# Performance work log

Hardware: AMD Instinct MI355X
Metric: run time of the kernel (lower is better)

Reference implementation:

```python
import jax, jax.numpy as jnp
import numpy as np

N_TOKENS = 100000
UNITS = 150  # CustomizeLSTMCell.TRANSITION_STATE_OUTPUTS_DIM


def setup_inputs() -> dict:
    key = jax.random.key(0)
    ks = jax.random.split(key, 9)
    f = lambda k, shape: jax.random.normal(k, shape, dtype=jnp.float32)
    return {
        "s_in": f(ks[0], (N_TOKENS, UNITS)),
        "s_out": f(ks[1], (N_TOKENS, UNITS)),
        "h_in": f(ks[2], (N_TOKENS, UNITS)),
        "h_out": f(ks[3], (N_TOKENS, UNITS)),
        "last_c": f(ks[4], (N_TOKENS, UNITS)),
        "w_in_input": f(ks[5], (UNITS, UNITS)) * 0.05,
        "w_out_input": f(ks[6], (UNITS, UNITS)) * 0.05,
        "u_in_input": f(ks[7], (UNITS, UNITS)) * 0.05,
        "u_out_input": f(ks[8], (UNITS, UNITS)) * 0.05,
    }


def reference(s_in, s_out, h_in, h_out, last_c,
              w_in_input, w_out_input, u_in_input, u_out_input):
    # Faithful to the source: all four gates use the *_input weights and no bias
    # (the original call() computes identical pre-activations for every gate).
    pre = (s_in @ w_in_input + s_out @ w_out_input
           + h_in @ u_in_input + h_out @ u_out_input)  # [N, H]
    gate = jax.nn.sigmoid(pre)
    # input_gate == output_gate == forget_gate == update_gate == gate
    cell_state = gate * last_c + gate * gate
    hidden_state = gate * jnp.tanh(cell_state)
    return hidden_state, cell_state
```

## Files before the change

### kernel.cpp

```cpp
#include <hip/hip_runtime.h>
#include <hip/hip_bf16.h>

typedef __attribute__((ext_vector_type(8))) short short8;
typedef __attribute__((ext_vector_type(4))) float f32x4;

#define NTOK   100000
#define H      150
#define NKS    20
#define BM     64
#define LBUF   18432
#define OUTOFF (NTOK * H)
#define AS1 __attribute__((address_space(1)))
#define AS3 __attribute__((address_space(3)))

__device__ __forceinline__ unsigned short f2bf(float f) {
    unsigned int u = __builtin_bit_cast(unsigned int, f);
    u = (u + 0x7FFFu + ((u >> 16) & 1u)) >> 16;
    return (unsigned short)u;
}

template<int N> __device__ __forceinline__ void vwait() {
    if constexpr (N == 6)       asm volatile("s_waitcnt vmcnt(6)" ::: "memory");
    else if constexpr (N == 4)  asm volatile("s_waitcnt vmcnt(4)" ::: "memory");
    else if constexpr (N == 23) asm volatile("s_waitcnt vmcnt(23)" ::: "memory");
    else if constexpr (N == 22) asm volatile("s_waitcnt vmcnt(22)" ::: "memory");
    else if constexpr (N == 20) asm volatile("s_waitcnt vmcnt(20)" ::: "memory");
    else                        asm volatile("s_waitcnt vmcnt(0)" ::: "memory");
}

__global__ void prep_w(const float* __restrict__ w_in, const float* __restrict__ w_out,
                       const float* __restrict__ u_in, const float* __restrict__ u_out,
                       unsigned short* __restrict__ wb) {
    int idx = blockIdx.x * 256 + threadIdx.x;
    if (idx >= NKS * 10 * 512) return;
    int j    = idx & 7;
    int lane = (idx >> 3) & 63;
    int n    = (idx >> 9) % 10;
    int ks   = idx / 5120;
    int seg  = ks / 5, s5 = ks % 5;
    int col  = n * 16 + (lane & 15);
    int p    = (lane >> 4) * 8 + j;
    int k2   = (s5 < 4) ? (s5 * 32 + p) : (118 + p);
    float v = 0.0f;
    if (col < H && !(s5 == 4 && p < 10)) {
        const float* W = (seg == 0) ? w_in : (seg == 1) ? w_out : (seg == 2) ? u_in : u_out;
        v = W[k2 * H + col];
    }
    wb[idx] = f2bf(v);
}

__global__ __launch_bounds__(512, 4) void lstm_fused(
        const float* __restrict__ s_in, const float* __restrict__ s_out,
        const float* __restrict__ h_in, const float* __restrict__ h_out,
        const float* __restrict__ last_c, const unsigned short* __restrict__ wb,
        float* __restrict__ out) {
    __shared__ __align__(16) char lds[4 * LBUF];

    const int t     = threadIdx.x;
    const int lane  = t & 63;
    const int wid   = t >> 6;
    const int waveM = wid >> 1;
    const int waveN = wid & 1;
    const int lrow  = lane & 15;
    const int lko   = lane >> 4;
    const int r0blk = blockIdx.x * BM;
    const bool cw3  = (wid < 2);

    const float* Xseg[4] = {s_in, s_out, h_in, h_out};

    f32x4 acc[5];
#pragma unroll
    for (int n = 0; n < 5; n++) acc[n] = (f32x4){0.f, 0.f, 0.f, 0.f};

    float lcv[4][5];

    auto stage = [&](int ks2) {
        char* lb = &lds[(ks2 & 3) * LBUF];
        const int s5 = ks2 % 5;
        const int sofs = (s5 < 4) ? s5 * 128 : 472;
        {
            const char* xb = (const char*)Xseg[ks2 / 5];
            int rowg = r0blk + wid * 8 + (lane >> 3);
            if (rowg > NTOK - 1) rowg = NTOK - 1;
            const int q = (lane & 7) ^ ((lane >> 3) & 7);
            const long go = (long)rowg * 600 + sofs + q * 16;
            __builtin_amdgcn_global_load_lds(
                (const AS1 void*)(xb + go),
                (AS3 void*)(lb + wid * 1024 + lane * 16), 16, 0, 0);
        }
        {
            const char* bsrc = (const char*)wb + (long)ks2 * 10240;
            __builtin_amdgcn_global_load_lds(
                (const AS1 void*)(bsrc + wid * 1024 + lane * 16),
                (AS3 void*)(lb + 8192 + wid * 1024 + lane * 16), 16, 0, 0);
            if (cw3)
                __builtin_amdgcn_global_load_lds(
                    (const AS1 void*)(bsrc + (8 + wid) * 1024 + lane * 16),
                    (AS3 void*)(lb + 8192 + (8 + wid) * 1024 + lane * 16), 16, 0, 0);
        }
    };

    auto compute = [&](int ks2) {
        const char* lb = &lds[(ks2 & 3) * LBUF];
        const int row = waveM * 16 + lrow;
        const int r7 = lrow & 7;
        const char* xr = lb + row * 128;
        f32x4 v0 = *(const f32x4*)(xr + ((((lko << 1) | 0) ^ r7) << 4));
        f32x4 v1 = *(const f32x4*)(xr + ((((lko << 1) | 1) ^ r7) << 4));
        short8 af;
        af[0] = (short)f2bf(v0[0]); af[1] = (short)f2bf(v0[1]);
        af[2] = (short)f2bf(v0[2]); af[3] = (short)f2bf(v0[3]);
        af[4] = (short)f2bf(v1[0]); af[5] = (short)f2bf(v1[1]);
        af[6] = (short)f2bf(v1[2]); af[7] = (short)f2bf(v1[3]);
        const char* br = lb + 8192 + (waveN * 5) * 1024 + lane * 16;
        __builtin_amdgcn_s_setprio(1);
#pragma unroll
        for (int n = 0; n < 5; n++) {
            short8 bf = *(const short8*)(br + n * 1024);
            acc[n] = __builtin_amdgcn_mfma_f32_16x16x32_bf16(af, bf, acc[n], 0, 0, 0);
        }
        __builtin_amdgcn_s_setprio(0);
    };

    stage(0); stage(1); stage(2);

#pragma unroll
    for (int ks = 0; ks < NKS; ks++) {
        if (ks < NKS - 2)       { if (cw3) vwait<6>();  else vwait<4>();  }
        else if (ks == NKS - 2) { if (cw3) vwait<23>(); else vwait<22>(); }
        else                    vwait<20>();
        __builtin_amdgcn_s_barrier();
        asm volatile("" ::: "memory");

        if (ks < NKS - 3) stage(ks + 3);

        if (ks == NKS - 3) {
#pragma unroll
            for (int r = 0; r < 4; r++) {
                int row = r0blk + waveM * 16 + lko * 4 + r;
                if (row > NTOK - 1) row = NTOK - 1;
#pragma unroll
                for (int n = 0; n < 5; n++) {
                    int col = waveN * 80 + n * 16 + lrow;
                    if (col >= H) col = 0;
                    lcv[r][n] = last_c[(long)row * H + col];
                }
            }
        }

        compute(ks);
    }

    vwait<0>();

#pragma unroll
    for (int r = 0; r < 4; r++) {
        const int row = r0blk + waveM * 16 + lko * 4 + r;
        if (row >= NTOK) continue;
        const long rb = (long)row * H;
#pragma unroll
        for (int n = 0; n < 5; n++) {
            const int col = waveN * 80 + n * 16 + lrow;
            if (col >= H) continue;
            float pre = acc[n][r];
            float e   = __expf(-pre);
            float g   = __builtin_amdgcn_rcpf(1.f + e);
            float cell = g * lcv[r][n] + g * g;
            float e2  = __expf(-2.f * cell);
            float th  = (1.f - e2) * __builtin_amdgcn_rcpf(1.f + e2);
            out[rb + col]          = g * th;
            out[OUTOFF + rb + col] = cell;
        }
    }
}

extern "C" void kernel_launch(void* const* d_in, const int* in_sizes, int n_in,
                              void* d_out, int out_size, void* d_ws, size_t ws_size,
                              hipStream_t stream) {
    const float* s_in   = (const float*)d_in[0];
    const float* s_out  = (const float*)d_in[1];
    const float* h_in   = (const float*)d_in[2];
    const float* h_out  = (const float*)d_in[3];
    const float* last_c = (const float*)d_in[4];
    const float* w_in   = (const float*)d_in[5];
    const float* w_out  = (const float*)d_in[6];
    const float* u_in   = (const float*)d_in[7];
    const float* u_out  = (const float*)d_in[8];

    unsigned short* wb = (unsigned short*)d_ws;
    float* out = (float*)d_out;

    prep_w<<<(NKS * 10 * 512 + 255) / 256, 256, 0, stream>>>(w_in, w_out, u_in, u_out, wb);

    const int nblocks = (NTOK + BM - 1) / BM;
    lstm_fused<<<nblocks, 512, 0, stream>>>(s_in, s_out, h_in, h_out, last_c, wb, out);
}
```

Measured before the change: 113.7 us.

## Double block tile to 128 rows with two M-subtiles per wave, triple-buffer LDS

Raises the block M tile from 64 to 128 rows so each wave computes two 16-row subtiles sharing each B fragment. The weight tile staged to LDS per k-step is therefore reused across twice as many rows. The LDS ring drops from four stages to three (prefetch distance 2) to fit the larger X tile, and the vmcnt wait counts are retuned to match. It trades a shallower pipeline, more accumulator and last_c registers, and half as many blocks (less occupancy and parallelism) for better B reuse and fewer blocks to schedule.

```diff
diff --git a/kernel.cpp b/kernel.cpp
--- a/kernel.cpp
+++ b/kernel.cpp
@@ -7,8 +7,9 @@
 #define NTOK   100000
 #define H      150
 #define NKS    20
-#define BM     64
-#define LBUF   18432
+#define BM     128
+#define XBYT   16384
+#define LBUF   26624
 #define OUTOFF (NTOK * H)
 #define AS1 __attribute__((address_space(1)))
 #define AS3 __attribute__((address_space(3)))
@@ -20,11 +21,11 @@
 }
 
 template<int N> __device__ __forceinline__ void vwait() {
-    if constexpr (N == 6)       asm volatile("s_waitcnt vmcnt(6)" ::: "memory");
-    else if constexpr (N == 4)  asm volatile("s_waitcnt vmcnt(4)" ::: "memory");
-    else if constexpr (N == 23) asm volatile("s_waitcnt vmcnt(23)" ::: "memory");
-    else if constexpr (N == 22) asm volatile("s_waitcnt vmcnt(22)" ::: "memory");
-    else if constexpr (N == 20) asm volatile("s_waitcnt vmcnt(20)" ::: "memory");
+    if constexpr (N == 4)       asm volatile("s_waitcnt vmcnt(4)" ::: "memory");
+    else if constexpr (N == 3)  asm volatile("s_waitcnt vmcnt(3)" ::: "memory");
+    else if constexpr (N == 44) asm volatile("s_waitcnt vmcnt(44)" ::: "memory");
+    else if constexpr (N == 43) asm volatile("s_waitcnt vmcnt(43)" ::: "memory");
+    else if constexpr (N == 40) asm volatile("s_waitcnt vmcnt(40)" ::: "memory");
     else                        asm volatile("s_waitcnt vmcnt(0)" ::: "memory");
 }
 
@@ -54,7 +55,7 @@
         const float* __restrict__ h_in, const float* __restrict__ h_out,
         const float* __restrict__ last_c, const unsigned short* __restrict__ wb,
         float* __restrict__ out) {
-    __shared__ __align__(16) char lds[4 * LBUF];
+    __shared__ __align__(16) char lds[3 * LBUF];
 
     const int t     = threadIdx.x;
     const int lane  = t & 63;
@@ -68,84 +69,94 @@
 
     const float* Xseg[4] = {s_in, s_out, h_in, h_out};
 
-    f32x4 acc[5];
-#pragma unroll
-    for (int n = 0; n < 5; n++) acc[n] = (f32x4){0.f, 0.f, 0.f, 0.f};
-
-    float lcv[4][5];
+    f32x4 acc[2][5];
+#pragma unroll
+    for (int m = 0; m < 2; m++)
+#pragma unroll
+        for (int n = 0; n < 5; n++) acc[m][n] = (f32x4){0.f, 0.f, 0.f, 0.f};
+
+    float lcv[2][4][5];
 
     auto stage = [&](int ks2) {
-        char* lb = &lds[(ks2 & 3) * LBUF];
+        char* lb = &lds[(ks2 % 3) * LBUF];
         const int s5 = ks2 % 5;
         const int sofs = (s5 < 4) ? s5 * 128 : 472;
-        {
-            const char* xb = (const char*)Xseg[ks2 / 5];
-            int rowg = r0blk + wid * 8 + (lane >> 3);
+        const char* xb = (const char*)Xseg[ks2 / 5];
+        const int q = (lane & 7) ^ ((lane >> 3) & 7);
+#pragma unroll
+        for (int h2 = 0; h2 < 2; h2++) {
+            const int c = wid + h2 * 8;
+            int rowg = r0blk + c * 8 + (lane >> 3);
             if (rowg > NTOK - 1) rowg = NTOK - 1;
-            const int q = (lane & 7) ^ ((lane >> 3) & 7);
             const long go = (long)rowg * 600 + sofs + q * 16;
             __builtin_amdgcn_global_load_lds(
                 (const AS1 void*)(xb + go),
-                (AS3 void*)(lb + wid * 1024 + lane * 16), 16, 0, 0);
-        }
-        {
-            const char* bsrc = (const char*)wb + (long)ks2 * 10240;
+                (AS3 void*)(lb + c * 1024 + lane * 16), 16, 0, 0);
+        }
+        const char* bsrc = (const char*)wb + (long)ks2 * 10240;
+        __builtin_amdgcn_global_load_lds(
+            (const AS1 void*)(bsrc + wid * 1024 + lane * 16),
+            (AS3 void*)(lb + XBYT + wid * 1024 + lane * 16), 16, 0, 0);
+        if (cw3)
             __builtin_amdgcn_global_load_lds(
-                (const AS1 void*)(bsrc + wid * 1024 + lane * 16),
-                (AS3 void*)(lb + 8192 + wid * 1024 + lane * 16), 16, 0, 0);
-            if (cw3)
-                __builtin_amdgcn_global_load_lds(
-                    (const AS1 void*)(bsrc + (8 + wid) * 1024 + lane * 16),
-                    (AS3 void*)(lb + 8192 + (8 + wid) * 1024 + lane * 16), 16, 0, 0);
-        }
+                (const AS1 void*)(bsrc + (8 + wid) * 1024 + lane * 16),
+                (AS3 void*)(lb + XBYT + (8 + wid) * 1024 + lane * 16), 16, 0, 0);
     };
 
     auto compute = [&](int ks2) {
-        const char* lb = &lds[(ks2 & 3) * LBUF];
-        const int row = waveM * 16 + lrow;
-        const int r7 = lrow & 7;
-        const char* xr = lb + row * 128;
-        f32x4 v0 = *(const f32x4*)(xr + ((((lko << 1) | 0) ^ r7) << 4));
-        f32x4 v1 = *(const f32x4*)(xr + ((((lko << 1) | 1) ^ r7) << 4));
-        short8 af;
-        af[0] = (short)f2bf(v0[0]); af[1] = (short)f2bf(v0[1]);
-        af[2] = (short)f2bf(v0[2]); af[3] = (short)f2bf(v0[3]);
-        af[4] = (short)f2bf(v1[0]); af[5] = (short)f2bf(v1[1]);
-        af[6] = (short)f2bf(v1[2]); af[7] = (short)f2bf(v1[3]);
-        const char* br = lb + 8192 + (waveN * 5) * 1024 + lane * 16;
+        const char* lb = &lds[(ks2 % 3) * LBUF];
+        const char* br = lb + XBYT + (waveN * 5) * 1024 + lane * 16;
+        short8 af[2];
+#pragma unroll
+        for (int m = 0; m < 2; m++) {
+            const int row = waveM * 32 + m * 16 + lrow;
+            const int r7 = row & 7;
+            const char* xr = lb + row * 128;
+            f32x4 v0 = *(const f32x4*)(xr + ((((lko << 1) | 0) ^ r7) << 4));
+            f32x4 v1 = *(const f32x4*)(xr + ((((lko << 1) | 1) ^ r7) << 4));
+            af[m][0] = (short)f2bf(v0[0]); af[m][1] = (short)f2bf(v0[1]);
+            af[m][2] = (short)f2bf(v0[2]); af[m][3] = (short)f2bf(v0[3]);
+            af[m][4] = (short)f2bf(v1[0]); af[m][5] = (short)f2bf(v1[1]);
+            af[m][6] = (short)f2bf(v1[2]); af[m][7] = (short)f2bf(v1[3]);
+        }
         __builtin_amdgcn_s_setprio(1);
 #pragma unroll
         for (int n = 0; n < 5; n++) {
             short8 bf = *(const short8*)(br + n * 1024);
-            acc[n] = __builtin_amdgcn_mfma_f32_16x16x32_bf16(af, bf, acc[n], 0, 0, 0);
+            acc[0][n] = __builtin_amdgcn_mfma_f32_16x16x32_bf16(af[0], bf, acc[0][n], 0, 0, 0);
+            acc[1][n] = __builtin_amdgcn_mfma_f32_16x16x32_bf16(af[1], bf, acc[1][n], 0, 0, 0);
         }
         __builtin_amdgcn_s_setprio(0);
     };
 
-    stage(0); stage(1); stage(2);
+    stage(0); stage(1);
 
 #pragma unroll
     for (int ks = 0; ks < NKS; ks++) {
-        if (ks < NKS - 2)       { if (cw3) vwait<6>();  else vwait<4>();  }
-        else if (ks == NKS - 2) { if (cw3) vwait<23>(); else vwait<22>(); }
-        else                    vwait<20>();
+        if (ks < NKS - 2)       { if (cw3) vwait<4>();  else vwait<3>();  }
+        else if (ks == NKS - 2) { if (cw3) vwait<44>(); else vwait<43>(); }
+        else                    vwait<40>();
         __builtin_amdgcn_s_barrier();
         asm volatile("" ::: "memory");
 
-        if (ks < NKS - 3) stage(ks + 3);
+        if (ks < NKS - 2) stage(ks + 2);
 
         if (ks == NKS - 3) {
-#pragma unroll
-            for (int r = 0; r < 4; r++) {
-                int row = r0blk + waveM * 16 + lko * 4 + r;
-                if (row > NTOK - 1) row = NTOK - 1;
-#pragma unroll
-                for (int n = 0; n < 5; n++) {
-                    int col = waveN * 80 + n * 16 + lrow;
-                    if (col >= H) col = 0;
-                    lcv[r][n] = last_c[(long)row * H + col];
+            __builtin_amdgcn_sched_barrier(0);
+#pragma unroll
+            for (int m = 0; m < 2; m++)
+#pragma unroll
+                for (int r = 0; r < 4; r++) {
+                    int row = r0blk + waveM * 32 + m * 16 + lko * 4 + r;
+                    if (row > NTOK - 1) row = NTOK - 1;
+#pragma unroll
+                    for (int n = 0; n < 5; n++) {
+                        int col = waveN * 80 + n * 16 + lrow;
+                        if (col >= H) col = 0;
+                        lcv[m][r][n] = last_c[(long)row * H + col];
+                    }
                 }
-            }
+            __builtin_amdgcn_sched_barrier(0);
         }
 
         compute(ks);
@@ -154,22 +165,25 @@
     vwait<0>();
 
 #pragma unroll
-    for (int r = 0; r < 4; r++) {
-        const int row = r0blk + waveM * 16 + lko * 4 + r;
-        if (row >= NTOK) continue;
-        const long rb = (long)row * H;
-#pragma unroll
-        for (int n = 0; n < 5; n++) {
-            const int col = waveN * 80 + n * 16 + lrow;
-            if (col >= H) continue;
-            float pre = acc[n][r];
-            float e   = __expf(-pre);
-            float g   = __builtin_amdgcn_rcpf(1.f + e);
-            float cell = g * lcv[r][n] + g * g;
-            float e2  = __expf(-2.f * cell);
-            float th  = (1.f - e2) * __builtin_amdgcn_rcpf(1.f + e2);
-            out[rb + col]          = g * th;
-            out[OUTOFF + rb + col] = cell;
+    for (int m = 0; m < 2; m++) {
+#pragma unroll
+        for (int r = 0; r < 4; r++) {
+            const int row = r0blk + waveM * 32 + m * 16 + lko * 4 + r;
+            if (row >= NTOK) continue;
+            const long rb = (long)row * H;
+#pragma unroll
+            for (int n = 0; n < 5; n++) {
+                const int col = waveN * 80 + n * 16 + lrow;
+                if (col >= H) continue;
+                float pre = acc[m][n][r];
+                float e   = __expf(-pre);
+                float g   = __builtin_amdgcn_rcpf(1.f + e);
+                float cell = g * lcv[m][r][n] + g * g;
+                float e2  = __expf(-2.f * cell);
+                float th  = (1.f - e2) * __builtin_amdgcn_rcpf(1.f + e2);
+                out[rb + col]          = g * th;
+                out[OUTOFF + rb + col] = cell;
+            }
         }
     }
 }
```

Result: slower. 122.1 us (+7.4%).

## Process two 64-row tiles per block with continuous cross-tile load pipeline

Applied to the files above, without the earlier changes.

Each block now handles 128 rows as two sequential 64-row tiles, running a single 40-step software pipeline. Loads for the second tile start while the first tile's last K-slices compute, and the first tile's epilogue overlaps in-flight prefetches. This halves the block count and amortizes pipeline fill and drain, at the cost of fewer blocks and more complex vmcnt accounting. The weight slices are reloaded for the second tile.

```diff
diff --git a/kernel.cpp b/kernel.cpp
--- a/kernel.cpp
+++ b/kernel.cpp
@@ -6,12 +6,12 @@
 
 #define NTOK   100000
 #define H      150
-#define NKS    20
-#define BM     64
+#define NSL    40
 #define LBUF   18432
 #define OUTOFF (NTOK * H)
 #define AS1 __attribute__((address_space(1)))
 #define AS3 __attribute__((address_space(3)))
+#define VWAIT(n) asm volatile("s_waitcnt vmcnt(" #n ")" ::: "memory")
 
 __device__ __forceinline__ unsigned short f2bf(float f) {
     unsigned int u = __builtin_bit_cast(unsigned int, f);
@@ -19,20 +19,11 @@
     return (unsigned short)u;
 }
 
-template<int N> __device__ __forceinline__ void vwait() {
-    if constexpr (N == 6)       asm volatile("s_waitcnt vmcnt(6)" ::: "memory");
-    else if constexpr (N == 4)  asm volatile("s_waitcnt vmcnt(4)" ::: "memory");
-    else if constexpr (N == 23) asm volatile("s_waitcnt vmcnt(23)" ::: "memory");
-    else if constexpr (N == 22) asm volatile("s_waitcnt vmcnt(22)" ::: "memory");
-    else if constexpr (N == 20) asm volatile("s_waitcnt vmcnt(20)" ::: "memory");
-    else                        asm volatile("s_waitcnt vmcnt(0)" ::: "memory");
-}
-
 __global__ void prep_w(const float* __restrict__ w_in, const float* __restrict__ w_out,
                        const float* __restrict__ u_in, const float* __restrict__ u_out,
                        unsigned short* __restrict__ wb) {
     int idx = blockIdx.x * 256 + threadIdx.x;
-    if (idx >= NKS * 10 * 512) return;
+    if (idx >= 20 * 10 * 512) return;
     int j    = idx & 7;
     int lane = (idx >> 3) & 63;
     int n    = (idx >> 9) % 10;
@@ -63,7 +54,7 @@
     const int waveN = wid & 1;
     const int lrow  = lane & 15;
     const int lko   = lane >> 4;
-    const int r0blk = blockIdx.x * BM;
+    const int r0blk = blockIdx.x * 128;
     const bool cw3  = (wid < 2);
 
     const float* Xseg[4] = {s_in, s_out, h_in, h_out};
@@ -74,34 +65,31 @@
 
     float lcv[4][5];
 
-    auto stage = [&](int ks2) {
-        char* lb = &lds[(ks2 & 3) * LBUF];
-        const int s5 = ks2 % 5;
+    auto stage = [&](int sl) {
+        char* lb = &lds[(sl & 3) * LBUF];
+        const int s5 = sl % 5;
         const int sofs = (s5 < 4) ? s5 * 128 : 472;
-        {
-            const char* xb = (const char*)Xseg[ks2 / 5];
-            int rowg = r0blk + wid * 8 + (lane >> 3);
-            if (rowg > NTOK - 1) rowg = NTOK - 1;
-            const int q = (lane & 7) ^ ((lane >> 3) & 7);
-            const long go = (long)rowg * 600 + sofs + q * 16;
+        const int tb = (sl >= 20) ? 64 : 0;
+        const char* xb = (const char*)Xseg[(sl % 20) / 5];
+        int rowg = r0blk + tb + wid * 8 + (lane >> 3);
+        if (rowg > NTOK - 1) rowg = NTOK - 1;
+        const int q = (lane & 7) ^ ((lane >> 3) & 7);
+        const long go = (long)rowg * 600 + sofs + q * 16;
+        __builtin_amdgcn_global_load_lds(
+            (const AS1 void*)(xb + go),
+            (AS3 void*)(lb + wid * 1024 + lane * 16), 16, 0, 0);
+        const char* bsrc = (const char*)wb + (long)(sl % 20) * 10240;
+        __builtin_amdgcn_global_load_lds(
+            (const AS1 void*)(bsrc + wid * 1024 + lane * 16),
+            (AS3 void*)(lb + 8192 + wid * 1024 + lane * 16), 16, 0, 0);
+        if (cw3)
             __builtin_amdgcn_global_load_lds(
-                (const AS1 void*)(xb + go),
-                (AS3 void*)(lb + wid * 1024 + lane * 16), 16, 0, 0);
-        }
-        {
-            const char* bsrc = (const char*)wb + (long)ks2 * 10240;
-            __builtin_amdgcn_global_load_lds(
-                (const AS1 void*)(bsrc + wid * 1024 + lane * 16),
-                (AS3 void*)(lb + 8192 + wid * 1024 + lane * 16), 16, 0, 0);
-            if (cw3)
-                __builtin_amdgcn_global_load_lds(
-                    (const AS1 void*)(bsrc + (8 + wid) * 1024 + lane * 16),
-                    (AS3 void*)(lb + 8192 + (8 + wid) * 1024 + lane * 16), 16, 0, 0);
-        }
-    };
-
-    auto compute = [&](int ks2) {
-        const char* lb = &lds[(ks2 & 3) * LBUF];
+                (const AS1 void*)(bsrc + (8 + wid) * 1024 + lane * 16),
+                (AS3 void*)(lb + 8192 + (8 + wid) * 1024 + lane * 16), 16, 0, 0);
+    };
+
+    auto compute = [&](int sl) {
+        const char* lb = &lds[(sl & 3) * LBUF];
         const int row = waveM * 16 + lrow;
         const int r7 = lrow & 7;
         const char* xr = lb + row * 128;
@@ -122,56 +110,76 @@
         __builtin_amdgcn_s_setprio(0);
     };
 
+    auto lcfetch = [&](int tb) {
+#pragma unroll
+        for (int r = 0; r < 4; r++) {
+            int row = r0blk + tb + waveM * 16 + lko * 4 + r;
+            if (row > NTOK - 1) row = NTOK - 1;
+#pragma unroll
+            for (int n = 0; n < 5; n++) {
+                int col = waveN * 80 + n * 16 + lrow;
+                if (col >= H) col = 0;
+                lcv[r][n] = last_c[(long)row * H + col];
+            }
+        }
+    };
+
+    auto epilog = [&](int tb) {
+#pragma unroll
+        for (int r = 0; r < 4; r++) {
+            const int row = r0blk + tb + waveM * 16 + lko * 4 + r;
+            if (row >= NTOK) continue;
+            const long rb = (long)row * H;
+#pragma unroll
+            for (int n = 0; n < 5; n++) {
+                const int col = waveN * 80 + n * 16 + lrow;
+                if (col >= H) continue;
+                float pre = acc[n][r];
+                float e   = __expf(-pre);
+                float g   = __builtin_amdgcn_rcpf(1.f + e);
+                float cell = g * lcv[r][n] + g * g;
+                float e2  = __expf(-2.f * cell);
+                float th  = (1.f - e2) * __builtin_amdgcn_rcpf(1.f + e2);
+                out[rb + col]          = g * th;
+                out[OUTOFF + rb + col] = cell;
+            }
+        }
+#pragma unroll
+        for (int n = 0; n < 5; n++) acc[n] = (f32x4){0.f, 0.f, 0.f, 0.f};
+    };
+
     stage(0); stage(1); stage(2);
 
 #pragma unroll
-    for (int ks = 0; ks < NKS; ks++) {
-        if (ks < NKS - 2)       { if (cw3) vwait<6>();  else vwait<4>();  }
-        else if (ks == NKS - 2) { if (cw3) vwait<23>(); else vwait<22>(); }
-        else                    vwait<20>();
+    for (int ks = 0; ks < NSL; ks++) {
+        if (ks == 18 || ks == 19)      { if (cw3) VWAIT(26); else VWAIT(24); }
+        else if (ks == 20)             {  }
+        else if (ks == 38)             { if (cw3) VWAIT(23); else VWAIT(22); }
+        else if (ks == 39)             { VWAIT(20); }
+        else                           { if (cw3) VWAIT(6);  else VWAIT(4);  }
         __builtin_amdgcn_s_barrier();
         asm volatile("" ::: "memory");
 
-        if (ks < NKS - 3) stage(ks + 3);
-
-        if (ks == NKS - 3) {
-#pragma unroll
-            for (int r = 0; r < 4; r++) {
-                int row = r0blk + waveM * 16 + lko * 4 + r;
-                if (row > NTOK - 1) row = NTOK - 1;
-#pragma unroll
-                for (int n = 0; n < 5; n++) {
-                    int col = waveN * 80 + n * 16 + lrow;
-                    if (col >= H) col = 0;
-                    lcv[r][n] = last_c[(long)row * H + col];
-                }
-            }
+        if (ks < NSL - 3) stage(ks + 3);
+
+        if (ks == 17 || ks == 37) {
+            __builtin_amdgcn_sched_barrier(0);
+            lcfetch(ks == 17 ? 0 : 64);
+            __builtin_amdgcn_sched_barrier(0);
         }
 
         compute(ks);
+
+        if (ks == 19) {
+            if (cw3) VWAIT(6); else VWAIT(4);
+            __builtin_amdgcn_sched_barrier(0);
+            epilog(0);
+            __builtin_amdgcn_sched_barrier(0);
+        }
     }
 
-    vwait<0>();
-
-#pragma unroll
-    for (int r = 0; r < 4; r++) {
-        const int row = r0blk + waveM * 16 + lko * 4 + r;
-        if (row >= NTOK) continue;
-        const long rb = (long)row * H;
-#pragma unroll
-        for (int n = 0; n < 5; n++) {
-            const int col = waveN * 80 + n * 16 + lrow;
-            if (col >= H) continue;
-            float pre = acc[n][r];
-            float e   = __expf(-pre);
-            float g   = __builtin_amdgcn_rcpf(1.f + e);
-            float cell = g * lcv[r][n] + g * g;
-            float e2  = __expf(-2.f * cell);
-            float th  = (1.f - e2) * __builtin_amdgcn_rcpf(1.f + e2);
-            out[rb + col]          = g * th;
-            out[OUTOFF + rb + col] = cell;
-        }
-    }
+    VWAIT(0);
+    epilog(64);
 }
 
 extern "C" void kernel_launch(void* const* d_in, const int* in_sizes, int n_in,
@@ -190,8 +198,8 @@
     unsigned short* wb = (unsigned short*)d_ws;
     float* out = (float*)d_out;
 
-    prep_w<<<(NKS * 10 * 512 + 255) / 256, 256, 0, stream>>>(w_in, w_out, u_in, u_out, wb);
-
-    const int nblocks = (NTOK + BM - 1) / BM;
+    prep_w<<<(20 * 10 * 512 + 255) / 256, 256, 0, stream>>>(w_in, w_out, u_in, u_out, wb);
+
+    const int nblocks = (NTOK + 127) / 128;
     lstm_fused<<<nblocks, 512, 0, stream>>>(s_in, s_out, h_in, h_out, last_c, wb, out);
 }
```

Measured after the change: 142.0 us. +24.9%, slower.

## Deepen LDS prefetch pipeline from 4 to 8 stages with occupancy cut

Applied to the files above, without the earlier changes.

Doubles the LDS ring buffer to eight slots and prefetches seven K-slices ahead instead of three. The vmcnt waits are recomputed for each iteration, and the last_c loads are fenced with sched_barriers. The aim is to keep more global loads in flight per block and hide memory latency in this bandwidth-bound fused GEMM+LSTM kernel. In exchange, the larger LDS footprint (about 147KB) and launch_bounds(512,2) reduce resident blocks per CU, which lowers occupancy-based latency hiding.

```diff
diff --git a/kernel.cpp b/kernel.cpp
--- a/kernel.cpp
+++ b/kernel.cpp
@@ -20,12 +20,20 @@
 }
 
 template<int N> __device__ __forceinline__ void vwait() {
-    if constexpr (N == 6)       asm volatile("s_waitcnt vmcnt(6)" ::: "memory");
-    else if constexpr (N == 4)  asm volatile("s_waitcnt vmcnt(4)" ::: "memory");
+    if constexpr (N == 21)      asm volatile("s_waitcnt vmcnt(21)" ::: "memory");
+    else if constexpr (N == 14) asm volatile("s_waitcnt vmcnt(14)" ::: "memory");
+    else if constexpr (N == 18) asm volatile("s_waitcnt vmcnt(18)" ::: "memory");
+    else if constexpr (N == 15) asm volatile("s_waitcnt vmcnt(15)" ::: "memory");
+    else if constexpr (N == 12) asm volatile("s_waitcnt vmcnt(12)" ::: "memory");
+    else if constexpr (N == 10) asm volatile("s_waitcnt vmcnt(10)" ::: "memory");
+    else if constexpr (N == 9)  asm volatile("s_waitcnt vmcnt(9)"  ::: "memory");
+    else if constexpr (N == 8)  asm volatile("s_waitcnt vmcnt(8)"  ::: "memory");
+    else if constexpr (N == 6)  asm volatile("s_waitcnt vmcnt(6)"  ::: "memory");
+    else if constexpr (N == 4)  asm volatile("s_waitcnt vmcnt(4)"  ::: "memory");
     else if constexpr (N == 23) asm volatile("s_waitcnt vmcnt(23)" ::: "memory");
     else if constexpr (N == 22) asm volatile("s_waitcnt vmcnt(22)" ::: "memory");
     else if constexpr (N == 20) asm volatile("s_waitcnt vmcnt(20)" ::: "memory");
-    else                        asm volatile("s_waitcnt vmcnt(0)" ::: "memory");
+    else                        asm volatile("s_waitcnt vmcnt(0)"  ::: "memory");
 }
 
 __global__ void prep_w(const float* __restrict__ w_in, const float* __restrict__ w_out,
@@ -49,12 +57,12 @@
     wb[idx] = f2bf(v);
 }
 
-__global__ __launch_bounds__(512, 4) void lstm_fused(
+__global__ __launch_bounds__(512, 2) void lstm_fused(
         const float* __restrict__ s_in, const float* __restrict__ s_out,
         const float* __restrict__ h_in, const float* __restrict__ h_out,
         const float* __restrict__ last_c, const unsigned short* __restrict__ wb,
         float* __restrict__ out) {
-    __shared__ __align__(16) char lds[4 * LBUF];
+    __shared__ __align__(16) char lds[8 * LBUF];
 
     const int t     = threadIdx.x;
     const int lane  = t & 63;
@@ -74,34 +82,30 @@
 
     float lcv[4][5];
 
-    auto stage = [&](int ks2) {
-        char* lb = &lds[(ks2 & 3) * LBUF];
-        const int s5 = ks2 % 5;
+    auto stage = [&](int sl) {
+        char* lb = &lds[(sl & 7) * LBUF];
+        const int s5 = sl % 5;
         const int sofs = (s5 < 4) ? s5 * 128 : 472;
-        {
-            const char* xb = (const char*)Xseg[ks2 / 5];
-            int rowg = r0blk + wid * 8 + (lane >> 3);
-            if (rowg > NTOK - 1) rowg = NTOK - 1;
-            const int q = (lane & 7) ^ ((lane >> 3) & 7);
-            const long go = (long)rowg * 600 + sofs + q * 16;
+        const char* xb = (const char*)Xseg[sl / 5];
+        int rowg = r0blk + wid * 8 + (lane >> 3);
+        if (rowg > NTOK - 1) rowg = NTOK - 1;
+        const int q = (lane & 7) ^ ((lane >> 3) & 7);
+        const long go = (long)rowg * 600 + sofs + q * 16;
+        __builtin_amdgcn_global_load_lds(
+            (const AS1 void*)(xb + go),
+            (AS3 void*)(lb + wid * 1024 + lane * 16), 16, 0, 0);
+        const char* bsrc = (const char*)wb + (long)sl * 10240;
+        __builtin_amdgcn_global_load_lds(
+            (const AS1 void*)(bsrc + wid * 1024 + lane * 16),
+            (AS3 void*)(lb + 8192 + wid * 1024 + lane * 16), 16, 0, 0);
+        if (cw3)
             __builtin_amdgcn_global_load_lds(
-                (const AS1 void*)(xb + go),
-                (AS3 void*)(lb + wid * 1024 + lane * 16), 16, 0, 0);
-        }
-        {
-            const char* bsrc = (const char*)wb + (long)ks2 * 10240;
-            __builtin_amdgcn_global_load_lds(
-                (const AS1 void*)(bsrc + wid * 1024 + lane * 16),
-                (AS3 void*)(lb + 8192 + wid * 1024 + lane * 16), 16, 0, 0);
-            if (cw3)
-                __builtin_amdgcn_global_load_lds(
-                    (const AS1 void*)(bsrc + (8 + wid) * 1024 + lane * 16),
-                    (AS3 void*)(lb + 8192 + (8 + wid) * 1024 + lane * 16), 16, 0, 0);
-        }
+                (const AS1 void*)(bsrc + (8 + wid) * 1024 + lane * 16),
+                (AS3 void*)(lb + 8192 + (8 + wid) * 1024 + lane * 16), 16, 0, 0);
     };
 
-    auto compute = [&](int ks2) {
-        const char* lb = &lds[(ks2 & 3) * LBUF];
+    auto compute = [&](int sl) {
+        const char* lb = &lds[(sl & 7) * LBUF];
         const int row = waveM * 16 + lrow;
         const int r7 = lrow & 7;
         const char* xr = lb + row * 128;
@@ -122,19 +126,25 @@
         __builtin_amdgcn_s_setprio(0);
     };
 
-    stage(0); stage(1); stage(2);
+    stage(0); stage(1); stage(2); stage(3); stage(4); stage(5); stage(6);
 
 #pragma unroll
     for (int ks = 0; ks < NKS; ks++) {
-        if (ks < NKS - 2)       { if (cw3) vwait<6>();  else vwait<4>();  }
-        else if (ks == NKS - 2) { if (cw3) vwait<23>(); else vwait<22>(); }
-        else                    vwait<20>();
+        if (ks <= 12)      { if (cw3) vwait<21>(); else vwait<14>(); }
+        else if (ks == 13) { if (cw3) vwait<18>(); else vwait<12>(); }
+        else if (ks == 14) { if (cw3) vwait<15>(); else vwait<10>(); }
+        else if (ks == 15) { if (cw3) vwait<12>(); else vwait<8>();  }
+        else if (ks == 16) { if (cw3) vwait<9>();  else vwait<6>();  }
+        else if (ks == 17) { if (cw3) vwait<6>();  else vwait<4>();  }
+        else if (ks == 18) { if (cw3) vwait<23>(); else vwait<22>(); }
+        else               { vwait<20>(); }
         __builtin_amdgcn_s_barrier();
         asm volatile("" ::: "memory");
 
-        if (ks < NKS - 3) stage(ks + 3);
-
-        if (ks == NKS - 3) {
+        if (ks <= 12) stage(ks + 7);
+
+        if (ks == 17) {
+            __builtin_amdgcn_sched_barrier(0);
 #pragma unroll
             for (int r = 0; r < 4; r++) {
                 int row = r0blk + waveM * 16 + lko * 4 + r;
@@ -146,6 +156,7 @@
                     lcv[r][n] = last_c[(long)row * H + col];
                 }
             }
+            __builtin_amdgcn_sched_barrier(0);
         }
 
         compute(ks);
```

Measured after the change: 117.3 us. 1.03x slower.
